# Optimization experiments

Measured on AMD Instinct MI355X. Metric: run time of the kernel, lower is better.

## Reference

```python
import jax, jax.numpy as jnp
import numpy as np

D_MODEL = 1024
NUM_HEADS = 16
D_K = D_MODEL // NUM_HEADS
THETA = 10000.0
BATCH, SEQ = 2, 2048


def _rope(xh, pos):
    # xh: (..., h, s, d_k), pos: (s,) int
    half = D_K // 2
    inv_freq = THETA ** (-jnp.arange(half, dtype=jnp.float32) * 2.0 / D_K)  # (half,)
    ang = pos.astype(jnp.float32)[:, None] * inv_freq[None, :]              # (s, half)
    cos, sin = jnp.cos(ang), jnp.sin(ang)
    x1 = xh[..., 0::2]  # (..., h, s, half)
    x2 = xh[..., 1::2]
    r1 = x1 * cos - x2 * sin
    r2 = x1 * sin + x2 * cos
    out = jnp.stack([r1, r2], axis=-1)            # (..., h, s, half, 2)
    return out.reshape(xh.shape)


def setup_inputs() -> dict:
    key = jax.random.key(0)
    k1, k2, k3 = jax.random.split(key, 3)
    scale_qkv = (6.0 / (3 * D_MODEL + D_MODEL)) ** 0.5  # xavier uniform bound
    scale_o = (6.0 / (2 * D_MODEL)) ** 0.5
    return {
        "x": jax.random.normal(k1, (BATCH, SEQ, D_MODEL), dtype=jnp.float32),
        "token_positions": jnp.arange(SEQ, dtype=jnp.int64 if jax.config.jax_enable_x64 else jnp.int32),
        "qkv_proj": jax.random.uniform(k2, (3 * D_MODEL, D_MODEL), jnp.float32, -scale_qkv, scale_qkv),
        "o_proj": jax.random.uniform(k3, (D_MODEL, D_MODEL), jnp.float32, -scale_o, scale_o),
    }


def reference(x, token_positions, qkv_proj, o_proj):
    # fused QKV projection: x @ qkv_proj^T
    qkv = jnp.einsum('bsd,ed->bse', x, qkv_proj)          # (b, s, 3*d_model)
    q, k, v = jnp.split(qkv, 3, axis=-1)

    def to_heads(t):
        b, s, _ = t.shape
        return t.reshape(b, s, NUM_HEADS, D_K).transpose(0, 2, 1, 3)  # (b, h, s, d_k)

    qh, kh, vh = to_heads(q), to_heads(k), to_heads(v)
    qh = _rope(qh, token_positions)
    kh = _rope(kh, token_positions)

    scores = jnp.einsum('bhqd,bhkd->bhqk', qh, kh) / (D_K ** 0.5)
    s = x.shape[-2]
    causal = jnp.tril(jnp.ones((s, s), dtype=bool))
    scores = jnp.where(causal, scores, -jnp.inf)
    attn = jax.nn.softmax(scores, axis=-1)
    out = jnp.einsum('bhqk,bhkd->bhqd', attn, vh)          # (b, h, s, d_k)
    out = out.transpose(0, 2, 1, 3).reshape(x.shape[0], s, D_MODEL)
    return jnp.einsum('bsd,od->bso', out, o_proj)
```

## Files before the change

### kernel.cpp

```cpp
#include <hip/hip_runtime.h>
#include <hip/hip_bf16.h>
#include <math.h>

typedef __bf16 bf16_t;
typedef __attribute__((ext_vector_type(2))) __bf16 bf16x2;
typedef __attribute__((ext_vector_type(4))) __bf16 bf16x4;
typedef __attribute__((ext_vector_type(8))) __bf16 bf16x8;
typedef __attribute__((ext_vector_type(4))) float f32x4;

#define BATCH  2
#define SEQ    2048
#define DMODEL 1024
#define NHEADS 16
#define DK     64

typedef const __attribute__((address_space(1))) void* gas_t;
typedef __attribute__((address_space(3))) void* las_t;

#define X_N (BATCH * SEQ * DMODEL)
#define W_N (3 * DMODEL * DMODEL)
#define O_N (DMODEL * DMODEL)

__global__ __launch_bounds__(256) void convert_kernel(
    const float* __restrict__ x, const float* __restrict__ w, const float* __restrict__ o,
    bf16_t* __restrict__ xb, bf16_t* __restrict__ wb, bf16_t* __restrict__ ob)
{
    const int gid = blockIdx.x * 256 + threadIdx.x;
    const float* src; bf16_t* dst; int base = gid * 8;
    if (base < X_N)                { src = x; dst = xb; }
    else if (base < X_N + W_N)     { src = w; dst = wb; base -= X_N; }
    else                           { src = o; dst = ob; base -= X_N + W_N; }
    const f32x4 lo = *(const f32x4*)(src + base);
    const f32x4 hi = *(const f32x4*)(src + base + 4);
    bf16x8 r;
    r[0] = (bf16_t)lo[0]; r[1] = (bf16_t)lo[1]; r[2] = (bf16_t)lo[2]; r[3] = (bf16_t)lo[3];
    r[4] = (bf16_t)hi[0]; r[5] = (bf16_t)hi[1]; r[6] = (bf16_t)hi[2]; r[7] = (bf16_t)hi[3];
    *(bf16x8*)(dst + base) = r;
}

__device__ __forceinline__ void gemm128_body(
    const bf16_t* __restrict__ A, const bf16_t* __restrict__ B,
    int rowBase, int colBase, bf16_t* ldsA, bf16_t* ldsB, f32x4 acc[4][4])
{
    const int tid  = threadIdx.x;
    const int lane = tid & 63;
    const int l15  = lane & 15, quad = lane >> 4;
    const int qr   = ((tid >> 6) >> 1) * 64;
    const int qc   = ((tid >> 6) & 1) * 64;

    const int c0 = tid, c1 = tid + 256;
    const int r0 = c0 >> 2, kc0 = (c0 & 3) * 8;
    const int r1 = c1 >> 2, kc1 = (c1 & 3) * 8;
    const bf16_t* ga0 = A + (size_t)(rowBase + r0) * DMODEL + kc0;
    const bf16_t* ga1 = A + (size_t)(rowBase + r1) * DMODEL + kc1;
    const bf16_t* gb0 = B + (size_t)(colBase + r0) * DMODEL + kc0;
    const bf16_t* gb1 = B + (size_t)(colBase + r1) * DMODEL + kc1;

    for (int k0 = 0; k0 < DMODEL; k0 += 32) {
        __syncthreads();
        __builtin_amdgcn_global_load_lds((gas_t)(ga0 + k0), (las_t)(ldsA + c0 * 8), 16, 0, 0);
        __builtin_amdgcn_global_load_lds((gas_t)(ga1 + k0), (las_t)(ldsA + c1 * 8), 16, 0, 0);
        __builtin_amdgcn_global_load_lds((gas_t)(gb0 + k0), (las_t)(ldsB + c0 * 8), 16, 0, 0);
        __builtin_amdgcn_global_load_lds((gas_t)(gb1 + k0), (las_t)(ldsB + c1 * 8), 16, 0, 0);
        __syncthreads();

        bf16x8 af[4], bfr[4];
#pragma unroll
        for (int i = 0; i < 4; ++i)
            af[i] = *(const bf16x8*)&ldsA[(qr + i * 16 + l15) * 32 + quad * 8];
#pragma unroll
        for (int j = 0; j < 4; ++j)
            bfr[j] = *(const bf16x8*)&ldsB[(qc + j * 16 + l15) * 32 + quad * 8];
#pragma unroll
        for (int i = 0; i < 4; ++i)
#pragma unroll
            for (int j = 0; j < 4; ++j)
                acc[i][j] = __builtin_amdgcn_mfma_f32_16x16x32_bf16(af[i], bfr[j], acc[i][j], 0, 0, 0);
    }
}

__global__ __launch_bounds__(256) void qkv_gemm_kernel(
    const bf16_t* __restrict__ x, const bf16_t* __restrict__ w,
    const int* __restrict__ pos,
    bf16_t* __restrict__ qo, bf16_t* __restrict__ ko, bf16_t* __restrict__ vt)
{
    __shared__ bf16_t ldsA[128 * 32];
    __shared__ bf16_t ldsB[128 * 32];
    const int bid = blockIdx.x;
    const int xcd = bid & 7, t = bid >> 3;
    const int xh  = xcd >> 2, yh = xcd & 3;
    const int bx  = xh * 12 + (t % 12);
    const int by  = yh * 8  + (t / 12);
    const int rowBase = by * 128;
    const int colBase = bx * 128;
    f32x4 acc[4][4] = {};
    gemm128_body(x, w, rowBase, colBase, ldsA, ldsB, acc);

    const int lane = threadIdx.x & 63;
    const int l15 = lane & 15, quad = lane >> 4;
    const int qr = ((threadIdx.x >> 6) >> 1) * 64;
    const int qc = ((threadIdx.x >> 6) & 1) * 64;
#pragma unroll
    for (int j = 0; j < 4; ++j) {
        const int col  = colBase + qc + j * 16 + l15;
        const int part = col >> 10;
        const int h    = (col & 1023) >> 6;
        const int d    = col & 63;
        bf16_t* op = (part == 0) ? qo : (part == 1) ? ko : vt;
        if (part < 2) {
            const float invf  = exp2f(-(float)(d >> 1) * 0.4152410118609203f);
            const float psign = (d & 1) ? 1.f : -1.f;
#pragma unroll
            for (int i = 0; i < 4; ++i) {
#pragma unroll
                for (int r = 0; r < 4; ++r) {
                    const int m = rowBase + qr + i * 16 + quad * 4 + r;
                    const int b = m >> 11;
                    const int s = m & (SEQ - 1);
                    const float ang = (float)pos[s] * invf;
                    const float sn_ = __sinf(ang);
                    const float c_  = __cosf(ang);
                    const float v = acc[i][j][r];
                    const float p = __shfl_xor(v, 1);
                    const float res = fmaf(p, psign * sn_, v * c_);
                    op[((size_t)(b * NHEADS + h) * SEQ + s) * DK + d] = (bf16_t)res;
                }
            }
        } else {
#pragma unroll
            for (int i = 0; i < 4; ++i) {
#pragma unroll
                for (int r = 0; r < 4; ++r) {
                    const int m = rowBase + qr + i * 16 + quad * 4 + r;
                    const int b = m >> 11;
                    const int s = m & (SEQ - 1);
                    const int sp = (s & ~63) | ((s & 15) << 2) | ((s >> 4) & 3);
                    op[(size_t)(b * NHEADS + h) * SEQ * DK + (size_t)d * SEQ + sp]
                        = (bf16_t)acc[i][j][r];
                }
            }
        }
    }
}

__global__ __launch_bounds__(256) void out_gemm_kernel(
    const bf16_t* __restrict__ a, const bf16_t* __restrict__ w, float* __restrict__ out)
{
    __shared__ bf16_t ldsA[2 * 128 * 64];
    __shared__ bf16_t ldsB[2 * 64 * 64];
    const int tid  = threadIdx.x;
    const int lane = tid & 63;
    const int l15  = lane & 15, quad = lane >> 4;
    const int l7   = l15 & 7;
    const int wv   = tid >> 6;
    const int bid = blockIdx.x;
    const int xcd = bid & 7, t = bid >> 3;
    const int xh  = xcd >> 2, yh = xcd & 3;
    const int bx  = xh * 8 + (t & 7);
    const int by  = yh * 8 + (t >> 3);
    const int rowBase = by * 128;
    const int colBase = bx * 64;

    const int sr   = tid >> 3;
    const int scol = ((tid & 7) ^ (sr & 7)) * 8;
    const bf16_t* ga = a + (size_t)(rowBase + sr) * DMODEL + scol;
    const bf16_t* gb = w + (size_t)(colBase + sr) * DMODEL + scol;
    const int dd = tid * 8;

#pragma unroll
    for (int u = 0; u < 4; ++u)
        __builtin_amdgcn_global_load_lds((gas_t)(ga + (size_t)u * 32 * DMODEL),
                                         (las_t)(ldsA + dd + u * 2048), 16, 0, 0);
#pragma unroll
    for (int u = 0; u < 2; ++u)
        __builtin_amdgcn_global_load_lds((gas_t)(gb + (size_t)u * 32 * DMODEL),
                                         (las_t)(ldsB + dd + u * 2048), 16, 0, 0);
    __syncthreads();

    f32x4 acc[2][4] = {};
    int buf = 0;
    for (int k0 = 0; k0 < DMODEL; k0 += 64) {
        if (k0 + 64 < DMODEL) {
            const int offA = (buf ^ 1) * 8192, offB = (buf ^ 1) * 4096;
#pragma unroll
            for (int u = 0; u < 4; ++u)
                __builtin_amdgcn_global_load_lds((gas_t)(ga + k0 + 64 + (size_t)u * 32 * DMODEL),
                                                 (las_t)(ldsA + offA + dd + u * 2048), 16, 0, 0);
#pragma unroll
            for (int u = 0; u < 2; ++u)
                __builtin_amdgcn_global_load_lds((gas_t)(gb + k0 + 64 + (size_t)u * 32 * DMODEL),
                                                 (las_t)(ldsB + offB + dd + u * 2048), 16, 0, 0);
        }
        const bf16_t* La = ldsA + buf * 8192;
        const bf16_t* Lb = ldsB + buf * 4096;
#pragma unroll
        for (int kk = 0; kk < 2; ++kk) {
            const int sw = ((kk * 4 + quad) ^ l7) * 8;
            bf16x8 af[2], bfr[4];
#pragma unroll
            for (int i = 0; i < 2; ++i)
                af[i] = *(const bf16x8*)&La[(wv * 32 + i * 16 + l15) * 64 + sw];
#pragma unroll
            for (int j = 0; j < 4; ++j)
                bfr[j] = *(const bf16x8*)&Lb[(j * 16 + l15) * 64 + sw];
#pragma unroll
            for (int i = 0; i < 2; ++i)
#pragma unroll
                for (int j = 0; j < 4; ++j)
                    acc[i][j] = __builtin_amdgcn_mfma_f32_16x16x32_bf16(af[i], bfr[j], acc[i][j], 0, 0, 0);
        }
        __syncthreads();
        buf ^= 1;
    }
#pragma unroll
    for (int i = 0; i < 2; ++i) {
#pragma unroll
        for (int r = 0; r < 4; ++r) {
            const int m = rowBase + wv * 32 + i * 16 + quad * 4 + r;
#pragma unroll
            for (int j = 0; j < 4; ++j)
                out[(size_t)m * DMODEL + colBase + j * 16 + l15] = acc[i][j][r];
        }
    }
}

__global__ __launch_bounds__(512) void attn_kernel(
    const bf16_t* __restrict__ Q, const bf16_t* __restrict__ K,
    const bf16_t* __restrict__ VT, bf16_t* __restrict__ AO)
{
    __shared__ bf16_t Kb[2][64 * 64];
    __shared__ bf16_t Vb[2][64 * 64];
    __shared__ bf16_t Pb[8][16 * 72];

    const int bh = blockIdx.x & 31;
    const int j  = blockIdx.x >> 5;
    const int qb = (j < 8) ? j : 23 - j;
    const int nt = 2 * qb + 2;

    const int tid  = threadIdx.x;
    const int wave = tid >> 6, lane = tid & 63;
    const int l15  = lane & 15, quad = lane >> 4;
    const int q0   = qb * 128 + wave * 16;
    const size_t hb = (size_t)bh * SEQ * DK;

    const int sr = tid >> 3;
    const int sc = ((tid & 7) ^ (sr & 7)) * 8;
    const int dd = tid * 8;

    bf16x8 aq0, aq1;
    {
        const bf16_t* qrow = Q + hb + (size_t)(q0 + l15) * DK + quad * 8;
        aq0 = *(const bf16x8*)qrow;
        aq1 = *(const bf16x8*)(qrow + 32);
#pragma unroll
        for (int i = 0; i < 8; ++i) {
            aq0[i] = (bf16_t)((float)aq0[i] * 0.125f);
            aq1[i] = (bf16_t)((float)aq1[i] * 0.125f);
        }
    }

    f32x4 oacc[4] = {};
    float lsum[4] = {};

    __builtin_amdgcn_global_load_lds((gas_t)(K  + hb + (size_t)sr * DK + sc),
                                     (las_t)(&Kb[0][dd]), 16, 0, 0);
    __builtin_amdgcn_global_load_lds((gas_t)(VT + hb + (size_t)sr * SEQ + sc),
                                     (las_t)(&Vb[0][dd]), 16, 0, 0);
    __syncthreads();

    const int swA = (quad ^ (l15 & 7)) * 8;
    const int swB = ((4 + quad) ^ (l15 & 7)) * 8;

    int buf = 0;
    for (int kb = 0; kb < nt; ++kb) {
        if (kb + 1 < nt) {
            const bf16_t* kg = K  + hb + (size_t)(kb + 1) * 64 * DK;
            const bf16_t* vg = VT + hb + (kb + 1) * 64;
            __builtin_amdgcn_global_load_lds((gas_t)(kg + (size_t)sr * DK + sc),
                                             (las_t)(&Kb[buf ^ 1][dd]), 16, 0, 0);
            __builtin_amdgcn_global_load_lds((gas_t)(vg + (size_t)sr * SEQ + sc),
                                             (las_t)(&Vb[buf ^ 1][dd]), 16, 0, 0);
        }

        const bool act = (kb * 64 <= q0 + 15);
        const bool nm  = (kb * 64 + 63 > q0);

        if (act) {
            bf16x8 kf0[4], kf1[4];
#pragma unroll
            for (int c = 0; c < 4; ++c) {
                kf0[c] = *(const bf16x8*)&Kb[buf][(c * 16 + l15) * 64 + swA];
                kf1[c] = *(const bf16x8*)&Kb[buf][(c * 16 + l15) * 64 + swB];
            }
            f32x4 sc4[4];
#pragma unroll
            for (int c = 0; c < 4; ++c) {
                f32x4 z = {};
                z = __builtin_amdgcn_mfma_f32_16x16x32_bf16(aq0, kf0[c], z, 0, 0, 0);
                z = __builtin_amdgcn_mfma_f32_16x16x32_bf16(aq1, kf1[c], z, 0, 0, 0);
                sc4[c] = z;
            }
#pragma unroll
            for (int r = 0; r < 4; ++r) {
                bf16x4 pr;
#pragma unroll
                for (int c = 0; c < 4; ++c) {
                    float s = sc4[c][r];
                    if (nm) {
                        const int key = kb * 64 + c * 16 + l15;
                        const int qa  = q0 + quad * 4 + r;
                        s = (key <= qa) ? s : -INFINITY;
                    }
                    const float p = __expf(s - 8.0f);
                    lsum[r] += p;
                    pr[c] = (bf16_t)p;
                }
                *(bf16x4*)&Pb[wave][(quad * 4 + r) * 72 + l15 * 4] = pr;
            }
            asm volatile("s_waitcnt lgkmcnt(0)" ::: "memory");

            const bf16x8 ap0 = *(const bf16x8*)&Pb[wave][l15 * 72 + quad * 8];
            const bf16x8 ap1 = *(const bf16x8*)&Pb[wave][l15 * 72 + 32 + quad * 8];
#pragma unroll
            for (int t = 0; t < 4; ++t) {
                const bf16x8 bv0 = *(const bf16x8*)&Vb[buf][(t * 16 + l15) * 64 + swA];
                const bf16x8 bv1 = *(const bf16x8*)&Vb[buf][(t * 16 + l15) * 64 + swB];
                oacc[t] = __builtin_amdgcn_mfma_f32_16x16x32_bf16(ap0, bv0, oacc[t], 0, 0, 0);
                oacc[t] = __builtin_amdgcn_mfma_f32_16x16x32_bf16(ap1, bv1, oacc[t], 0, 0, 0);
            }
        }

        __syncthreads();
        buf ^= 1;
    }

    const int b = bh >> 4, h = bh & 15;
    float inv[4];
#pragma unroll
    for (int r = 0; r < 4; ++r) {
        float s = lsum[r];
        s += __shfl_xor(s, 1);
        s += __shfl_xor(s, 2);
        s += __shfl_xor(s, 4);
        s += __shfl_xor(s, 8);
        inv[r] = 1.0f / s;
    }
#pragma unroll
    for (int t = 0; t < 4; ++t)
#pragma unroll
        for (int r = 0; r < 4; ++r) {
            const int qa = q0 + quad * 4 + r;
            AO[(size_t)(b * SEQ + qa) * DMODEL + h * 64 + t * 16 + l15] =
                (bf16_t)(oacc[t][r] * inv[r]);
        }
}

extern "C" void kernel_launch(void* const* d_in, const int* in_sizes, int n_in,
                              void* d_out, int out_size, void* d_ws, size_t ws_size,
                              hipStream_t stream) {
    (void)in_sizes; (void)n_in; (void)out_size; (void)ws_size;
    const float* x    = (const float*)d_in[0];
    const int*   pos  = (const int*)d_in[1];
    const float* qkvw = (const float*)d_in[2];
    const float* ow   = (const float*)d_in[3];
    float* out = (float*)d_out;

    const size_t HEAD_ELEMS = (size_t)BATCH * NHEADS * SEQ * DK;
    bf16_t* Qw  = (bf16_t*)d_ws;
    bf16_t* Kw  = Qw + HEAD_ELEMS;
    bf16_t* Vt  = Kw + HEAD_ELEMS;
    bf16_t* AO  = Vt + HEAD_ELEMS;
    bf16_t* xb  = AO;
    bf16_t* wb  = AO + X_N;
    bf16_t* ob  = wb + W_N;

    convert_kernel<<<dim3(4096), 256, 0, stream>>>(x, qkvw, ow, xb, wb, ob);
    qkv_gemm_kernel<<<dim3(768), 256, 0, stream>>>(xb, wb, pos, Qw, Kw, Vt);
    attn_kernel<<<dim3(512), 512, 0, stream>>>(Qw, Kw, Vt, AO);
    out_gemm_kernel<<<dim3(512), 256, 0, stream>>>(AO, ob, out);
}
```

Baseline: 190.3 us.

## Rewrite QKV GEMM with 256x256 tiles, double-buffered LDS and XOR swizzle

Replaces the 128x128, K=32 single-buffered QKV GEMM with a 512-thread 256x256 tile over K=64 steps. The next K-slice is prefetched into a second LDS buffer while the current one is consumed, and an XOR swizzle is applied to the LDS layout to avoid bank conflicts. This aims to raise arithmetic intensity and overlap global loads with MFMA. The trade-off is a grid of only 192 blocks on a GPU with many CUs, 128KB of LDS per block and 128 accumulator floats per thread, which risks low occupancy and poor CU utilization.

```diff
diff --git a/kernel.cpp b/kernel.cpp
--- a/kernel.cpp
+++ b/kernel.cpp
@@ -38,83 +38,94 @@
     *(bf16x8*)(dst + base) = r;
 }
 
-__device__ __forceinline__ void gemm128_body(
-    const bf16_t* __restrict__ A, const bf16_t* __restrict__ B,
-    int rowBase, int colBase, bf16_t* ldsA, bf16_t* ldsB, f32x4 acc[4][4])
-{
-    const int tid  = threadIdx.x;
-    const int lane = tid & 63;
-    const int l15  = lane & 15, quad = lane >> 4;
-    const int qr   = ((tid >> 6) >> 1) * 64;
-    const int qc   = ((tid >> 6) & 1) * 64;
-
-    const int c0 = tid, c1 = tid + 256;
-    const int r0 = c0 >> 2, kc0 = (c0 & 3) * 8;
-    const int r1 = c1 >> 2, kc1 = (c1 & 3) * 8;
-    const bf16_t* ga0 = A + (size_t)(rowBase + r0) * DMODEL + kc0;
-    const bf16_t* ga1 = A + (size_t)(rowBase + r1) * DMODEL + kc1;
-    const bf16_t* gb0 = B + (size_t)(colBase + r0) * DMODEL + kc0;
-    const bf16_t* gb1 = B + (size_t)(colBase + r1) * DMODEL + kc1;
-
-    for (int k0 = 0; k0 < DMODEL; k0 += 32) {
-        __syncthreads();
-        __builtin_amdgcn_global_load_lds((gas_t)(ga0 + k0), (las_t)(ldsA + c0 * 8), 16, 0, 0);
-        __builtin_amdgcn_global_load_lds((gas_t)(ga1 + k0), (las_t)(ldsA + c1 * 8), 16, 0, 0);
-        __builtin_amdgcn_global_load_lds((gas_t)(gb0 + k0), (las_t)(ldsB + c0 * 8), 16, 0, 0);
-        __builtin_amdgcn_global_load_lds((gas_t)(gb1 + k0), (las_t)(ldsB + c1 * 8), 16, 0, 0);
-        __syncthreads();
-
-        bf16x8 af[4], bfr[4];
-#pragma unroll
-        for (int i = 0; i < 4; ++i)
-            af[i] = *(const bf16x8*)&ldsA[(qr + i * 16 + l15) * 32 + quad * 8];
-#pragma unroll
-        for (int j = 0; j < 4; ++j)
-            bfr[j] = *(const bf16x8*)&ldsB[(qc + j * 16 + l15) * 32 + quad * 8];
-#pragma unroll
-        for (int i = 0; i < 4; ++i)
-#pragma unroll
-            for (int j = 0; j < 4; ++j)
-                acc[i][j] = __builtin_amdgcn_mfma_f32_16x16x32_bf16(af[i], bfr[j], acc[i][j], 0, 0, 0);
-    }
-}
-
-__global__ __launch_bounds__(256) void qkv_gemm_kernel(
+__global__ __launch_bounds__(512) void qkv_gemm_kernel(
     const bf16_t* __restrict__ x, const bf16_t* __restrict__ w,
     const int* __restrict__ pos,
     bf16_t* __restrict__ qo, bf16_t* __restrict__ ko, bf16_t* __restrict__ vt)
 {
-    __shared__ bf16_t ldsA[128 * 32];
-    __shared__ bf16_t ldsB[128 * 32];
+    __shared__ bf16_t ldsA[2 * 256 * 64];
+    __shared__ bf16_t ldsB[2 * 256 * 64];
+
+    const int tid  = threadIdx.x;
+    const int lane = tid & 63;
+    const int l15  = lane & 15, quad = lane >> 4;
+    const int l7   = l15 & 7;
+    const int wv   = tid >> 6;
+    const int wr   = wv >> 2;
+    const int wc   = wv & 3;
+
     const int bid = blockIdx.x;
     const int xcd = bid & 7, t = bid >> 3;
-    const int xh  = xcd >> 2, yh = xcd & 3;
-    const int bx  = xh * 12 + (t % 12);
-    const int by  = yh * 8  + (t / 12);
-    const int rowBase = by * 128;
-    const int colBase = bx * 128;
-    f32x4 acc[4][4] = {};
-    gemm128_body(x, w, rowBase, colBase, ldsA, ldsB, acc);
-
-    const int lane = threadIdx.x & 63;
-    const int l15 = lane & 15, quad = lane >> 4;
-    const int qr = ((threadIdx.x >> 6) >> 1) * 64;
-    const int qc = ((threadIdx.x >> 6) & 1) * 64;
-#pragma unroll
-    for (int j = 0; j < 4; ++j) {
-        const int col  = colBase + qc + j * 16 + l15;
-        const int part = col >> 10;
-        const int h    = (col & 1023) >> 6;
-        const int d    = col & 63;
-        bf16_t* op = (part == 0) ? qo : (part == 1) ? ko : vt;
-        if (part < 2) {
+    const int rh  = xcd >> 1, ch = xcd & 1;
+    const int bx  = ch * 6 + (t % 6);
+    const int by  = rh * 4 + (t / 6);
+    const int rowBase = by * 256;
+    const int colBase = bx * 256;
+
+    const int sr   = tid >> 3;
+    const int scol = ((tid & 7) ^ (sr & 7)) * 8;
+    const bf16_t* ga = x + (size_t)(rowBase + sr) * DMODEL + scol;
+    const bf16_t* gb = w + (size_t)(colBase + sr) * DMODEL + scol;
+    const int dd = tid * 8;
+
+#pragma unroll
+    for (int u = 0; u < 4; ++u) {
+        __builtin_amdgcn_global_load_lds((gas_t)(ga + (size_t)u * 64 * DMODEL),
+                                         (las_t)(ldsA + dd + u * 4096), 16, 0, 0);
+        __builtin_amdgcn_global_load_lds((gas_t)(gb + (size_t)u * 64 * DMODEL),
+                                         (las_t)(ldsB + dd + u * 4096), 16, 0, 0);
+    }
+    __syncthreads();
+
+    f32x4 acc[8][4] = {};
+    int buf = 0;
+    for (int k0 = 0; k0 < DMODEL; k0 += 64) {
+        if (k0 + 64 < DMODEL) {
+            const int off = (buf ^ 1) * 16384;
+#pragma unroll
+            for (int u = 0; u < 4; ++u) {
+                __builtin_amdgcn_global_load_lds((gas_t)(ga + k0 + 64 + (size_t)u * 64 * DMODEL),
+                                                 (las_t)(ldsA + off + dd + u * 4096), 16, 0, 0);
+                __builtin_amdgcn_global_load_lds((gas_t)(gb + k0 + 64 + (size_t)u * 64 * DMODEL),
+                                                 (las_t)(ldsB + off + dd + u * 4096), 16, 0, 0);
+            }
+        }
+        const bf16_t* La = ldsA + buf * 16384;
+        const bf16_t* Lb = ldsB + buf * 16384;
+#pragma unroll
+        for (int kk = 0; kk < 2; ++kk) {
+            const int sw = ((kk * 4 + quad) ^ l7) * 8;
+            bf16x8 bfr[4];
+#pragma unroll
+            for (int j = 0; j < 4; ++j)
+                bfr[j] = *(const bf16x8*)&Lb[(wc * 64 + j * 16 + l15) * 64 + sw];
+#pragma unroll
+            for (int i = 0; i < 8; ++i) {
+                const bf16x8 af = *(const bf16x8*)&La[(wr * 128 + i * 16 + l15) * 64 + sw];
+#pragma unroll
+                for (int j = 0; j < 4; ++j)
+                    acc[i][j] = __builtin_amdgcn_mfma_f32_16x16x32_bf16(af, bfr[j], acc[i][j], 0, 0, 0);
+            }
+        }
+        __syncthreads();
+        buf ^= 1;
+    }
+
+    const int colW = colBase + wc * 64;
+    const int part = colW >> 10;
+    const int h    = (colW & 1023) >> 6;
+    bf16_t* op = (part == 0) ? qo : (part == 1) ? ko : vt;
+    if (part < 2) {
+#pragma unroll
+        for (int j = 0; j < 4; ++j) {
+            const int d = j * 16 + l15;
             const float invf  = exp2f(-(float)(d >> 1) * 0.4152410118609203f);
             const float psign = (d & 1) ? 1.f : -1.f;
 #pragma unroll
-            for (int i = 0; i < 4; ++i) {
+            for (int i = 0; i < 8; ++i) {
 #pragma unroll
                 for (int r = 0; r < 4; ++r) {
-                    const int m = rowBase + qr + i * 16 + quad * 4 + r;
+                    const int m = rowBase + wr * 128 + i * 16 + quad * 4 + r;
                     const int b = m >> 11;
                     const int s = m & (SEQ - 1);
                     const float ang = (float)pos[s] * invf;
@@ -126,12 +137,16 @@
                     op[((size_t)(b * NHEADS + h) * SEQ + s) * DK + d] = (bf16_t)res;
                 }
             }
-        } else {
-#pragma unroll
-            for (int i = 0; i < 4; ++i) {
+        }
+    } else {
+#pragma unroll
+        for (int j = 0; j < 4; ++j) {
+            const int d = j * 16 + l15;
+#pragma unroll
+            for (int i = 0; i < 8; ++i) {
 #pragma unroll
                 for (int r = 0; r < 4; ++r) {
-                    const int m = rowBase + qr + i * 16 + quad * 4 + r;
+                    const int m = rowBase + wr * 128 + i * 16 + quad * 4 + r;
                     const int b = m >> 11;
                     const int s = m & (SEQ - 1);
                     const int sp = (s & ~63) | ((s & 15) << 2) | ((s >> 4) & 3);
@@ -375,7 +390,7 @@
     bf16_t* ob  = wb + W_N;
 
     convert_kernel<<<dim3(4096), 256, 0, stream>>>(x, qkvw, ow, xb, wb, ob);
-    qkv_gemm_kernel<<<dim3(768), 256, 0, stream>>>(xb, wb, pos, Qw, Kw, Vt);
+    qkv_gemm_kernel<<<dim3(192), 512, 0, stream>>>(xb, wb, pos, Qw, Kw, Vt);
     attn_kernel<<<dim3(512), 512, 0, stream>>>(Qw, Kw, Vt, AO);
     out_gemm_kernel<<<dim3(512), 256, 0, stream>>>(AO, ob, out);
 }
```

Result: faster. 186.0 us (-2.2%).

## Shrink attention query tile to 64 rows and drop K/V double buffering

Applied to the files above, without the earlier changes.

The attention kernel now uses 256-thread blocks with 64 query rows each and launches 1024 blocks instead of 512. Block-to-query-tile assignment becomes a four-way zigzag to balance causal work. Because every wave in a block now needs every key tile up to the diagonal, the per-wave activity check is dropped. The K/V double buffer is replaced by a single buffer loaded synchronously each iteration with two barriers, which lowers LDS use and should raise occupancy. The cost is that load latency is no longer overlapped with compute, and K/V tiles are re-read by twice as many blocks.

```diff
diff --git a/kernel.cpp b/kernel.cpp
--- a/kernel.cpp
+++ b/kernel.cpp
@@ -224,28 +224,32 @@
     }
 }
 
-__global__ __launch_bounds__(512) void attn_kernel(
+__global__ __launch_bounds__(256) void attn_kernel(
     const bf16_t* __restrict__ Q, const bf16_t* __restrict__ K,
     const bf16_t* __restrict__ VT, bf16_t* __restrict__ AO)
 {
-    __shared__ bf16_t Kb[2][64 * 64];
-    __shared__ bf16_t Vb[2][64 * 64];
-    __shared__ bf16_t Pb[8][16 * 72];
+    __shared__ bf16_t Kb[64 * 64];
+    __shared__ bf16_t Vb[64 * 64];
+    __shared__ bf16_t Pb[4][16 * 72];
 
     const int bh = blockIdx.x & 31;
     const int j  = blockIdx.x >> 5;
-    const int qb = (j < 8) ? j : 23 - j;
-    const int nt = 2 * qb + 2;
+    const int lo = j & 7, hi = j >> 3;
+    const int qb = (hi == 0) ? lo
+                 : (hi == 1) ? (31 - lo)
+                 : (hi == 2) ? (8 + lo)
+                 :             (23 - lo);
+    const int nt = qb + 1;
 
     const int tid  = threadIdx.x;
     const int wave = tid >> 6, lane = tid & 63;
     const int l15  = lane & 15, quad = lane >> 4;
-    const int q0   = qb * 128 + wave * 16;
+    const int q0   = qb * 64 + wave * 16;
     const size_t hb = (size_t)bh * SEQ * DK;
 
-    const int sr = tid >> 3;
-    const int sc = ((tid & 7) ^ (sr & 7)) * 8;
-    const int dd = tid * 8;
+    const int r0 = tid >> 3;
+    const int sc = ((tid & 7) ^ (r0 & 7)) * 8;
+    const int dd0 = tid * 8, dd1 = (tid + 256) * 8;
 
     bf16x8 aq0, aq1;
     {
@@ -261,77 +265,65 @@
 
     f32x4 oacc[4] = {};
     float lsum[4] = {};
-
-    __builtin_amdgcn_global_load_lds((gas_t)(K  + hb + (size_t)sr * DK + sc),
-                                     (las_t)(&Kb[0][dd]), 16, 0, 0);
-    __builtin_amdgcn_global_load_lds((gas_t)(VT + hb + (size_t)sr * SEQ + sc),
-                                     (las_t)(&Vb[0][dd]), 16, 0, 0);
-    __syncthreads();
-
     const int swA = (quad ^ (l15 & 7)) * 8;
     const int swB = ((4 + quad) ^ (l15 & 7)) * 8;
 
-    int buf = 0;
     for (int kb = 0; kb < nt; ++kb) {
-        if (kb + 1 < nt) {
-            const bf16_t* kg = K  + hb + (size_t)(kb + 1) * 64 * DK;
-            const bf16_t* vg = VT + hb + (kb + 1) * 64;
-            __builtin_amdgcn_global_load_lds((gas_t)(kg + (size_t)sr * DK + sc),
-                                             (las_t)(&Kb[buf ^ 1][dd]), 16, 0, 0);
-            __builtin_amdgcn_global_load_lds((gas_t)(vg + (size_t)sr * SEQ + sc),
-                                             (las_t)(&Vb[buf ^ 1][dd]), 16, 0, 0);
-        }
-
-        const bool act = (kb * 64 <= q0 + 15);
-        const bool nm  = (kb * 64 + 63 > q0);
-
-        if (act) {
-            bf16x8 kf0[4], kf1[4];
+        __syncthreads();
+        {
+            const bf16_t* kg = K  + hb + (size_t)kb * 64 * DK + (size_t)r0 * DK  + sc;
+            const bf16_t* vg = VT + hb + kb * 64 + (size_t)r0 * SEQ + sc;
+            __builtin_amdgcn_global_load_lds((gas_t)kg,              (las_t)(&Kb[dd0]), 16, 0, 0);
+            __builtin_amdgcn_global_load_lds((gas_t)(kg + 32 * DK),  (las_t)(&Kb[dd1]), 16, 0, 0);
+            __builtin_amdgcn_global_load_lds((gas_t)vg,              (las_t)(&Vb[dd0]), 16, 0, 0);
+            __builtin_amdgcn_global_load_lds((gas_t)(vg + 32 * SEQ), (las_t)(&Vb[dd1]), 16, 0, 0);
+        }
+        __syncthreads();
+
+        const bool nm = (kb == qb);
+
+        bf16x8 kf0[4], kf1[4];
+#pragma unroll
+        for (int c = 0; c < 4; ++c) {
+            kf0[c] = *(const bf16x8*)&Kb[(c * 16 + l15) * 64 + swA];
+            kf1[c] = *(const bf16x8*)&Kb[(c * 16 + l15) * 64 + swB];
+        }
+        f32x4 sc4[4];
+#pragma unroll
+        for (int c = 0; c < 4; ++c) {
+            f32x4 z = {};
+            z = __builtin_amdgcn_mfma_f32_16x16x32_bf16(aq0, kf0[c], z, 0, 0, 0);
+            z = __builtin_amdgcn_mfma_f32_16x16x32_bf16(aq1, kf1[c], z, 0, 0, 0);
+            sc4[c] = z;
+        }
+#pragma unroll
+        for (int r = 0; r < 4; ++r) {
+            bf16x4 pr;
 #pragma unroll
             for (int c = 0; c < 4; ++c) {
-                kf0[c] = *(const bf16x8*)&Kb[buf][(c * 16 + l15) * 64 + swA];
-                kf1[c] = *(const bf16x8*)&Kb[buf][(c * 16 + l15) * 64 + swB];
+                float s = sc4[c][r];
+                if (nm) {
+                    const int key = kb * 64 + c * 16 + l15;
+                    const int qa  = q0 + quad * 4 + r;
+                    s = (key <= qa) ? s : -INFINITY;
+                }
+                const float p = __expf(s - 8.0f);
+                lsum[r] += p;
+                pr[c] = (bf16_t)p;
             }
-            f32x4 sc4[4];
-#pragma unroll
-            for (int c = 0; c < 4; ++c) {
-                f32x4 z = {};
-                z = __builtin_amdgcn_mfma_f32_16x16x32_bf16(aq0, kf0[c], z, 0, 0, 0);
-                z = __builtin_amdgcn_mfma_f32_16x16x32_bf16(aq1, kf1[c], z, 0, 0, 0);
-                sc4[c] = z;
-            }
-#pragma unroll
-            for (int r = 0; r < 4; ++r) {
-                bf16x4 pr;
-#pragma unroll
-                for (int c = 0; c < 4; ++c) {
-                    float s = sc4[c][r];
-                    if (nm) {
-                        const int key = kb * 64 + c * 16 + l15;
-                        const int qa  = q0 + quad * 4 + r;
-                        s = (key <= qa) ? s : -INFINITY;
-                    }
-                    const float p = __expf(s - 8.0f);
-                    lsum[r] += p;
-                    pr[c] = (bf16_t)p;
-                }
-                *(bf16x4*)&Pb[wave][(quad * 4 + r) * 72 + l15 * 4] = pr;
-            }
-            asm volatile("s_waitcnt lgkmcnt(0)" ::: "memory");
-
-            const bf16x8 ap0 = *(const bf16x8*)&Pb[wave][l15 * 72 + quad * 8];
-            const bf16x8 ap1 = *(const bf16x8*)&Pb[wave][l15 * 72 + 32 + quad * 8];
-#pragma unroll
-            for (int t = 0; t < 4; ++t) {
-                const bf16x8 bv0 = *(const bf16x8*)&Vb[buf][(t * 16 + l15) * 64 + swA];
-                const bf16x8 bv1 = *(const bf16x8*)&Vb[buf][(t * 16 + l15) * 64 + swB];
-                oacc[t] = __builtin_amdgcn_mfma_f32_16x16x32_bf16(ap0, bv0, oacc[t], 0, 0, 0);
-                oacc[t] = __builtin_amdgcn_mfma_f32_16x16x32_bf16(ap1, bv1, oacc[t], 0, 0, 0);
-            }
-        }
-
-        __syncthreads();
-        buf ^= 1;
+            *(bf16x4*)&Pb[wave][(quad * 4 + r) * 72 + l15 * 4] = pr;
+        }
+        asm volatile("s_waitcnt lgkmcnt(0)" ::: "memory");
+
+        const bf16x8 ap0 = *(const bf16x8*)&Pb[wave][l15 * 72 + quad * 8];
+        const bf16x8 ap1 = *(const bf16x8*)&Pb[wave][l15 * 72 + 32 + quad * 8];
+#pragma unroll
+        for (int t = 0; t < 4; ++t) {
+            const bf16x8 bv0 = *(const bf16x8*)&Vb[(t * 16 + l15) * 64 + swA];
+            const bf16x8 bv1 = *(const bf16x8*)&Vb[(t * 16 + l15) * 64 + swB];
+            oacc[t] = __builtin_amdgcn_mfma_f32_16x16x32_bf16(ap0, bv0, oacc[t], 0, 0, 0);
+            oacc[t] = __builtin_amdgcn_mfma_f32_16x16x32_bf16(ap1, bv1, oacc[t], 0, 0, 0);
+        }
     }
 
     const int b = bh >> 4, h = bh & 15;
@@ -376,6 +368,6 @@
 
     convert_kernel<<<dim3(4096), 256, 0, stream>>>(x, qkvw, ow, xb, wb, ob);
     qkv_gemm_kernel<<<dim3(768), 256, 0, stream>>>(xb, wb, pos, Qw, Kw, Vt);
-    attn_kernel<<<dim3(512), 512, 0, stream>>>(Qw, Kw, Vt, AO);
+    attn_kernel<<<dim3(1024), 256, 0, stream>>>(Qw, Kw, Vt, AO);
     out_gemm_kernel<<<dim3(512), 256, 0, stream>>>(AO, ob, out);
 }
```

Result: faster. 183.0 us (-3.8%).
